# Kernel optimization log

Hardware: AMD Instinct MI355X
Metric: run time of the kernel (lower is better)

## Reference

```python
import jax, jax.numpy as jnp
import numpy as np

IN_DIM = 64
HIDDEN = 128
NUM_LAYERS = 2
N_NODES = 10000
N_EDGES = 160000
N_GRAPHS = 32


def _lin_params(key, fan_in, fan_out):
    kw, kb = jax.random.split(key)
    s = 1.0 / np.sqrt(fan_in)
    W = jax.random.uniform(kw, (fan_in, fan_out), jnp.float32, -s, s)
    b = jax.random.uniform(kb, (fan_out,), jnp.float32, -s, s)
    return W, b


def setup_inputs() -> dict:
    key = jax.random.key(0)
    ks = jax.random.split(key, 24)
    H = HIDDEN
    inp = {}
    inp["x1"] = jax.random.normal(ks[0], (N_NODES, IN_DIM), jnp.float32)
    inp["edge_index1"] = jax.random.randint(ks[1], (2, N_EDGES), 0, N_NODES)
    inp["batch1"] = jnp.sort(jax.random.randint(ks[2], (N_NODES,), 0, N_GRAPHS))
    inp["x2"] = jax.random.normal(ks[3], (N_NODES, IN_DIM), jnp.float32)
    inp["edge_index2"] = jax.random.randint(ks[4], (2, N_EDGES), 0, N_NODES)
    inp["batch2"] = jnp.sort(jax.random.randint(ks[5], (N_NODES,), 0, N_GRAPHS))
    # embedding: Linear(in_dim -> hidden)
    inp["W_emb"], inp["b_emb"] = _lin_params(ks[6], IN_DIM, H)
    # per-layer GEMBConv params, stacked over layers
    mW1, mb1, mW2, mb2, uW1, ub1, uW2, ub2 = [], [], [], [], [], [], [], []
    for l in range(NUM_LAYERS):
        k = jax.random.split(ks[7 + l], 4)
        W, b = _lin_params(k[0], 2 * H, 2 * H); mW1.append(W); mb1.append(b)
        W, b = _lin_params(k[1], 2 * H, 2 * H); mW2.append(W); mb2.append(b)
        W, b = _lin_params(k[2], 3 * H, 2 * H); uW1.append(W); ub1.append(b)
        W, b = _lin_params(k[3], 2 * H, H); uW2.append(W); ub2.append(b)
    inp["msg_W1"] = jnp.stack(mW1); inp["msg_b1"] = jnp.stack(mb1)
    inp["msg_W2"] = jnp.stack(mW2); inp["msg_b2"] = jnp.stack(mb2)
    inp["upd_W1"] = jnp.stack(uW1); inp["upd_b1"] = jnp.stack(ub1)
    inp["upd_W2"] = jnp.stack(uW2); inp["upd_b2"] = jnp.stack(ub2)
    # readout: node_net Linear(H -> 2H) (use_gate doubles), graph_net Linear(H -> H)
    inp["node_W"], inp["node_b"] = _lin_params(ks[20], H, 2 * H)
    inp["graph_W"], inp["graph_b"] = _lin_params(ks[21], H, H)
    return inp


def _genet_branch(x, edge_index, batch, W_emb, b_emb,
                  msg_W1, msg_b1, msg_W2, msg_b2,
                  upd_W1, upd_b1, upd_W2, upd_b2,
                  node_W, node_b, graph_W, graph_b):
    H = HIDDEN
    h = x @ W_emb + b_emb  # [N, H]
    tgt, src = edge_index[0], edge_index[1]
    for l in range(NUM_LAYERS):
        # gather-concat: (x[src], x[tgt]) -> [E, 2H]
        mi = jnp.concatenate([h[src], h[tgt]], axis=-1)
        m = jax.nn.relu(mi @ msg_W1[l] + msg_b1[l]) @ msg_W2[l] + msg_b2[l]
        agg = jax.ops.segment_sum(m, tgt, num_segments=N_NODES)  # [N, 2H]
        ui = jnp.concatenate([agg, h], axis=-1)  # [N, 3H]
        u = jax.nn.relu(ui @ upd_W1[l] + upd_b1[l]) @ upd_W2[l] + upd_b2[l]
        h = h + u  # residual node update
    nx = h @ node_W + node_b  # [N, 2H]
    gates = jax.nn.sigmoid(nx[:, :H])
    v = nx[:, H:] * gates
    g = jax.ops.segment_sum(v, batch, num_segments=N_GRAPHS)  # sum pool
    return g @ graph_W + graph_b  # [G, H]


def reference(x1, edge_index1, batch1, x2, edge_index2, batch2,
              W_emb, b_emb, msg_W1, msg_b1, msg_W2, msg_b2,
              upd_W1, upd_b1, upd_W2, upd_b2,
              node_W, node_b, graph_W, graph_b):
    args = (W_emb, b_emb, msg_W1, msg_b1, msg_W2, msg_b2,
            upd_W1, upd_b1, upd_W2, upd_b2, node_W, node_b, graph_W, graph_b)
    embed1 = _genet_branch(x1, edge_index1, batch1, *args)
    embed2 = _genet_branch(x2, edge_index2, batch2, *args)
    return (embed1, embed2)
```

## Files before the change

### kernel.cpp

```cpp
#include <hip/hip_runtime.h>

typedef unsigned short u16;
typedef __bf16 bf16x8 __attribute__((ext_vector_type(8)));
typedef float f32x4 __attribute__((ext_vector_type(4)));
typedef unsigned short u16x8 __attribute__((ext_vector_type(8)));

constexpr int NN  = 10000;
constexpr int NE  = 160000;
constexpr int NG  = 32;
constexpr int HD  = 128;

constexpr size_t WT_PQ   = 0;
constexpr size_t WT_U1C  = 262144;
constexpr size_t WT_UPD2 = 655360;
constexpr size_t WT_NODE = 786432;
constexpr size_t WT_EMB  = 851968;
constexpr size_t OFF_C2  = 868352;
constexpr size_t OFF_DEG = 870400;
constexpr size_t OFF_ST  = 950400;
constexpr size_t OFF_CUR = 1030464;
constexpr size_t OFF_SRC = 1110464;
constexpr size_t OFF_HB  = 2390464;
constexpr size_t OFF_PQ  = 7510464;
constexpr size_t OFF_S   = 27990464;
constexpr size_t OFF_G   = 38230464;
constexpr size_t OFF_XB  = 38263232;

#define LSTR 40

__device__ inline u16 f2b(float f) {
  unsigned int u = __float_as_uint(f);
  unsigned int r = u + 0x7fffu + ((u >> 16) & 1u);
  return (u16)(r >> 16);
}
__device__ inline float b2f(u16 u) { return __uint_as_float(((unsigned int)u) << 16); }

__global__ __launch_bounds__(256) void k_prep(
    const float* msgW1, const float* msgW2, const float* updW1,
    const float* updW2, const float* nodeW, const float* msgb2,
    const float* W_emb, const float* x1, const float* x2,
    u16* tpq, u16* tu1c, u16* t4, u16* t5, u16* temb, u16* xb,
    float* c2, int* deg, float* g) {
  int idx = blockIdx.x * 256 + threadIdx.x;
  if (idx < 131072) {
    int l = idx >> 16, r = idx & 65535, n = r >> 7, k = r & 127;
    int row = (n < 256) ? k : (128 + k);
    tpq[idx] = f2b(msgW1[l * 65536 + row * 256 + (n & 255)]);
  }
  if (idx < 65536) {
    int l = idx >> 15, r = idx & 32767, n = r >> 7, k = r & 127;
    tu1c[l * 98304 + n * 384 + 256 + k] = f2b(updW1[l * 98304 + (256 + k) * 256 + n]);
    int n2 = (idx & 32767) >> 8, k2 = idx & 255;
    t4[idx] = f2b(updW2[(idx >> 15) * 32768 + (k2 << 7) + n2]);
  }
  if (idx < 32768) {
    int n = idx >> 7, k = idx & 127;
    t5[idx] = f2b(nodeW[(k << 8) + n]);
  }
  if (idx < 512) {
    int l = idx >> 8, n = idx & 255;
    const float* b2 = msgb2 + l * 256;
    const float* U1 = updW1 + l * 98304 + n;
    float a = 0.f;
    for (int c = 0; c < 256; c++) a += b2[c] * U1[c * 256];
    c2[idx] = a;
  }
  if (idx < 2 * NN) deg[idx] = 0;
  if (idx < 2 * NG * 128) g[idx] = 0.f;
  if (idx >= 131072 && idx < 262144) {
    int j = idx - 131072;
    int l = j >> 16, r = j & 65535, k = r >> 8, n = r & 255;
    const float* w2p = msgW2 + l * 65536 + k * 256;
    const float* u1p = updW1 + l * 98304 + n;
    float a = 0.f;
    for (int c = 0; c < 256; c++) a += w2p[c] * u1p[c * 256];
    tu1c[l * 98304 + n * 384 + k] = f2b(a);
  }
  if (idx >= 262144 && idx < 270336) {
    int j = idx - 262144;
    int n = j >> 6, k = j & 63;
    temb[j] = f2b(W_emb[(k << 7) + n]);
  }
  if (idx >= 270336 && idx < 1550336) {
    int j = idx - 270336;
    int br = j >= NN * 64;
    int jj = br ? j - NN * 64 : j;
    const float* x = br ? x2 : x1;
    xb[(size_t)br * NN * 64 + jj] = f2b(x[jj]);
  }
}

__global__ __launch_bounds__(256) void k_deg(const int* ei0, const int* ei1, int* deg) {
  int br = blockIdx.z;
  int e = blockIdx.x * 256 + threadIdx.x;
  if (e >= NE) return;
  const int* tgt = br ? ei1 : ei0;
  atomicAdd(deg + br * NN + tgt[e], 1);
}

__global__ __launch_bounds__(256) void k_scan(const int* deg, int* starts, int* cursor) {
  int br = blockIdx.z;
  const int* d = deg + br * NN;
  int* st = starts + br * (NN + 8);
  int* cu = cursor + br * NN;
  __shared__ int part[257];
  int t = threadIdx.x;
  int c0 = t * 40;
  int s = 0;
  for (int i = 0; i < 40; i++) if (c0 + i < NN) s += d[c0 + i];
  part[t] = s;
  __syncthreads();
  if (t == 0) {
    int run = 0;
    for (int i = 0; i < 256; i++) { int v = part[i]; part[i] = run; run += v; }
    part[256] = run;
  }
  __syncthreads();
  int run = part[t];
  for (int i = 0; i < 40; i++) {
    int n = c0 + i;
    if (n < NN) { st[n] = run; cu[n] = run; run += d[n]; }
  }
  if (t == 255) st[NN] = part[256];
}

__global__ __launch_bounds__(256) void k_scatter(const int* ei0, const int* ei1,
                                                 int* cursor, int* srcs) {
  int br = blockIdx.z;
  int e = blockIdx.x * 256 + threadIdx.x;
  if (e >= NE) return;
  const int* ei = br ? ei1 : ei0;
  int t = ei[e], s = ei[NE + e];
  int pos = atomicAdd(cursor + br * NN + t, 1);
  srcs[br * NE + pos] = s;
}

__device__ __forceinline__ void pq_from_lhb(
    const u16* lhb, const u16* wq, u16* PQ, int m0, int wave, int lane) {
  const int q = lane >> 4, lr = lane & 15;
  f32x4 a3[2][8];
#pragma unroll
  for (int i = 0; i < 2; i++)
#pragma unroll
    for (int j = 0; j < 8; j++) a3[i][j] = (f32x4){0.f, 0.f, 0.f, 0.f};
  bf16x8 bcur[8], bnxt[8];
#pragma unroll
  for (int i = 0; i < 8; i++)
    bcur[i] = *(const bf16x8*)(wq + (size_t)(wave * 128 + i * 16 + lr) * 128 + q * 8);
#pragma unroll
  for (int k0 = 0; k0 < 128; k0 += 32) {
    if (k0 + 32 < 128) {
#pragma unroll
      for (int i = 0; i < 8; i++)
        bnxt[i] = *(const bf16x8*)(wq + (size_t)(wave * 128 + i * 16 + lr) * 128 + k0 + 32 + q * 8);
    }
    bf16x8 af[2];
#pragma unroll
    for (int i = 0; i < 2; i++)
      af[i] = *(const bf16x8*)&lhb[(i * 16 + lr) * 136 + k0 + q * 8];
#pragma unroll
    for (int mi = 0; mi < 2; mi++)
#pragma unroll
      for (int ni = 0; ni < 8; ni++)
        a3[mi][ni] = __builtin_amdgcn_mfma_f32_16x16x32_bf16(af[mi], bcur[ni], a3[mi][ni], 0, 0, 0);
#pragma unroll
    for (int i = 0; i < 8; i++) bcur[i] = bnxt[i];
  }
#pragma unroll
  for (int mi = 0; mi < 2; mi++)
#pragma unroll
    for (int rg = 0; rg < 4; rg++) {
      int grow = m0 + mi * 16 + q * 4 + rg;
      if (grow >= NN) continue;
#pragma unroll
      for (int ni = 0; ni < 8; ni++) {
        int col = wave * 128 + ni * 16 + lr;
        PQ[(size_t)grow * 512 + col] = f2b(a3[mi][ni][rg]);
      }
    }
}

__global__ __launch_bounds__(256) void k_embed(
    const u16* xb_all, const u16* wemb, const float* b,
    u16* hb_all, const u16* wpq0, u16* PQ_all) {
  const int br = blockIdx.z;
  const int tid = threadIdx.x;
  const int lane = tid & 63, wave = tid >> 6;
  const int q = lane >> 4, lr = lane & 15;
  const int m0 = blockIdx.x * 32;

  __shared__ alignas(16) u16 lx[32 * 72];
  __shared__ alignas(16) u16 lhb[32 * 136];

  const u16* xb = xb_all + (size_t)br * NN * 64;
  {
    int r = tid >> 3, kc = (tid & 7) * 8;
    int gr = m0 + r;
    u16x8 v = {0, 0, 0, 0, 0, 0, 0, 0};
    if (gr < NN) v = *(const u16x8*)(xb + (size_t)gr * 64 + kc);
    *(u16x8*)&lx[r * 72 + kc] = v;
  }
  __syncthreads();

  const int wn = wave * 32;
  f32x4 acc[2][2];
#pragma unroll
  for (int i = 0; i < 2; i++)
#pragma unroll
    for (int j = 0; j < 2; j++) acc[i][j] = (f32x4){0.f, 0.f, 0.f, 0.f};

#pragma unroll
  for (int k0 = 0; k0 < 64; k0 += 32) {
    bf16x8 af[2], bfr[2];
#pragma unroll
    for (int i = 0; i < 2; i++)
      af[i] = *(const bf16x8*)&lx[(i * 16 + lr) * 72 + k0 + q * 8];
#pragma unroll
    for (int i = 0; i < 2; i++)
      bfr[i] = *(const bf16x8*)(wemb + (size_t)(wn + i * 16 + lr) * 64 + k0 + q * 8);
#pragma unroll
    for (int mi = 0; mi < 2; mi++)
#pragma unroll
      for (int ni = 0; ni < 2; ni++)
        acc[mi][ni] = __builtin_amdgcn_mfma_f32_16x16x32_bf16(af[mi], bfr[ni], acc[mi][ni], 0, 0, 0);
  }

  u16* hbB = hb_all + (size_t)br * NN * HD;
#pragma unroll
  for (int mi = 0; mi < 2; mi++)
#pragma unroll
    for (int rg = 0; rg < 4; rg++) {
      int lrow = mi * 16 + q * 4 + rg;
      int gr = m0 + lrow;
#pragma unroll
      for (int ni = 0; ni < 2; ni++) {
        int col = wn + ni * 16 + lr;
        if (gr < NN) {
          u16 bv = f2b(acc[mi][ni][rg] + b[col]);
          hbB[(size_t)gr * HD + col] = bv;
          lhb[lrow * 136 + col] = bv;
        } else {
          lhb[lrow * 136 + col] = 0;
        }
      }
    }
  __syncthreads();
  pq_from_lhb(lhb, wpq0, PQ_all + (size_t)br * NN * 512, m0, wave, lane);
}

__global__ __launch_bounds__(256) void k_edge(const u16* PQ, const int* starts,
                                              const int* srcs, const float* b1, u16* S) {
  int br = blockIdx.z;
  int node = blockIdx.x * 4 + (threadIdx.x >> 6);
  int lane = threadIdx.x & 63;
  int half = lane >> 5;
  int c0 = (lane & 31) * 8;
  const u16* PQb = PQ + (size_t)br * NN * 512;
  const int* st = starts + br * (NN + 8);
  const int* sr = srcs + br * NE;
  u16x8 qr = *(const u16x8*)(PQb + (size_t)node * 512 + 256 + c0);
  float qv[8], acc[8];
#pragma unroll
  for (int j = 0; j < 8; j++) { qv[j] = b2f(qr[j]) + b1[c0 + j]; acc[j] = 0.f; }
  int e0 = st[node], e1 = st[node + 1];
  int mid = e0 + ((e1 - e0 + 1) >> 1);
  int e = half ? mid : e0;
  int ee = half ? e1 : mid;
  for (; e + 3 < ee; e += 4) {
    int s0 = sr[e], s1 = sr[e + 1], s2 = sr[e + 2], s3 = sr[e + 3];
    u16x8 p0 = *(const u16x8*)(PQb + (size_t)s0 * 512 + c0);
    u16x8 p1 = *(const u16x8*)(PQb + (size_t)s1 * 512 + c0);
    u16x8 p2 = *(const u16x8*)(PQb + (size_t)s2 * 512 + c0);
    u16x8 p3 = *(const u16x8*)(PQb + (size_t)s3 * 512 + c0);
#pragma unroll
    for (int j = 0; j < 8; j++) {
      float v0 = b2f(p0[j]) + qv[j];
      float v1 = b2f(p1[j]) + qv[j];
      float v2 = b2f(p2[j]) + qv[j];
      float v3 = b2f(p3[j]) + qv[j];
      acc[j] += (v0 > 0.f ? v0 : 0.f) + (v1 > 0.f ? v1 : 0.f)
              + (v2 > 0.f ? v2 : 0.f) + (v3 > 0.f ? v3 : 0.f);
    }
  }
  for (; e + 1 < ee; e += 2) {
    int s0 = sr[e], s1 = sr[e + 1];
    u16x8 p0 = *(const u16x8*)(PQb + (size_t)s0 * 512 + c0);
    u16x8 p1 = *(const u16x8*)(PQb + (size_t)s1 * 512 + c0);
#pragma unroll
    for (int j = 0; j < 8; j++) {
      float v0 = b2f(p0[j]) + qv[j];
      float v1 = b2f(p1[j]) + qv[j];
      acc[j] += (v0 > 0.f ? v0 : 0.f) + (v1 > 0.f ? v1 : 0.f);
    }
  }
  if (e < ee) {
    int s0 = sr[e];
    u16x8 p0 = *(const u16x8*)(PQb + (size_t)s0 * 512 + c0);
#pragma unroll
    for (int j = 0; j < 8; j++) {
      float v0 = b2f(p0[j]) + qv[j];
      acc[j] += (v0 > 0.f ? v0 : 0.f);
    }
  }
#pragma unroll
  for (int j = 0; j < 8; j++) acc[j] += __shfl_xor(acc[j], 32);
  if (half == 0) {
    u16x8 o;
#pragma unroll
    for (int j = 0; j < 8; j++) o[j] = f2b(acc[j]);
    *(u16x8*)(S + (size_t)br * NN * 256 + (size_t)node * 256 + c0) = o;
  }
}

__global__ __launch_bounds__(256, 4) void k_upd(
    const u16* S_all, u16* hb_all, const u16* w1c, const float* b1u,
    const float* c2l, const int* deg_all, const u16* w2, const float* b2u,
    int mode, const u16* wpq_next, u16* PQ_all,
    const u16* wnode, const float* nb, const int* b0v, const int* b1v, float* g) {
  const int br = blockIdx.z;
  const int tid = threadIdx.x;
  const int lane = tid & 63, wave = tid >> 6;
  const int q = lane >> 4, lr = lane & 15;
  const int m0 = blockIdx.x * 32;

  __shared__ alignas(16) u16 lA[32 * 392];
  __shared__ alignas(16) u16 lhb[32 * 136];
  __shared__ int sbat[32];
  u16* lU = lA;

  const u16* S = S_all + (size_t)br * NN * 256;
  u16* hb = hb_all + (size_t)br * NN * 128;

  for (int c = tid; c < 1536; c += 256) {
    int r = c / 48, kc = (c % 48) * 8;
    int gr = m0 + r;
    u16x8 v = {0, 0, 0, 0, 0, 0, 0, 0};
    if (gr < NN) {
      if (kc < 256) v = *(const u16x8*)(S + (size_t)gr * 256 + kc);
      else          v = *(const u16x8*)(hb + (size_t)gr * 128 + (kc - 256));
    }
    *(u16x8*)&lA[r * 392 + kc] = v;
  }
  if (mode == 1 && tid < 32) {
    const int* batch = br ? b1v : b0v;
    int n = m0 + tid;
    sbat[tid] = (n < NN) ? batch[n] : -1;
  }
  __syncthreads();

  const int wn = wave * 64;
  f32x4 acc[2][4];
#pragma unroll
  for (int i = 0; i < 2; i++)
#pragma unroll
    for (int j = 0; j < 4; j++) acc[i][j] = (f32x4){0.f, 0.f, 0.f, 0.f};

  bf16x8 bcur[4], bnxt[4];
#pragma unroll
  for (int i = 0; i < 4; i++)
    bcur[i] = *(const bf16x8*)(w1c + (size_t)(wn + i * 16 + lr) * 384 + q * 8);
#pragma unroll
  for (int k0 = 0; k0 < 384; k0 += 32) {
    if (k0 + 32 < 384) {
#pragma unroll
      for (int i = 0; i < 4; i++)
        bnxt[i] = *(const bf16x8*)(w1c + (size_t)(wn + i * 16 + lr) * 384 + k0 + 32 + q * 8);
    }
    bf16x8 af[2];
#pragma unroll
    for (int i = 0; i < 2; i++)
      af[i] = *(const bf16x8*)&lA[(i * 16 + lr) * 392 + k0 + q * 8];
#pragma unroll
    for (int mi = 0; mi < 2; mi++)
#pragma unroll
      for (int ni = 0; ni < 4; ni++)
        acc[mi][ni] = __builtin_amdgcn_mfma_f32_16x16x32_bf16(af[mi], bcur[ni], acc[mi][ni], 0, 0, 0);
#pragma unroll
    for (int i = 0; i < 4; i++) bcur[i] = bnxt[i];
  }
  __syncthreads();

  const int* deg = deg_all + br * NN;
#pragma unroll
  for (int mi = 0; mi < 2; mi++)
#pragma unroll
    for (int rg = 0; rg < 4; rg++) {
      int row = mi * 16 + q * 4 + rg;
      int gr = m0 + row;
      float d = (gr < NN) ? (float)deg[gr] : 0.f;
#pragma unroll
      for (int ni = 0; ni < 4; ni++) {
        int col = wn + ni * 16 + lr;
        float v = acc[mi][ni][rg] + b1u[col] + d * c2l[col];
        if (v < 0.f) v = 0.f;
        lU[row * 272 + col] = f2b(v);
      }
    }
  __syncthreads();

  const int wn2 = wave * 32;
  f32x4 acc2[2][2];
#pragma unroll
  for (int i = 0; i < 2; i++)
#pragma unroll
    for (int j = 0; j < 2; j++) acc2[i][j] = (f32x4){0.f, 0.f, 0.f, 0.f};

  bf16x8 b2c[2], b2n[2];
#pragma unroll
  for (int i = 0; i < 2; i++)
    b2c[i] = *(const bf16x8*)(w2 + (size_t)(wn2 + i * 16 + lr) * 256 + q * 8);
#pragma unroll
  for (int k0 = 0; k0 < 256; k0 += 32) {
    if (k0 + 32 < 256) {
#pragma unroll
      for (int i = 0; i < 2; i++)
        b2n[i] = *(const bf16x8*)(w2 + (size_t)(wn2 + i * 16 + lr) * 256 + k0 + 32 + q * 8);
    }
    bf16x8 af[2];
#pragma unroll
    for (int i = 0; i < 2; i++)
      af[i] = *(const bf16x8*)&lU[(i * 16 + lr) * 272 + k0 + q * 8];
#pragma unroll
    for (int mi = 0; mi < 2; mi++)
#pragma unroll
      for (int ni = 0; ni < 2; ni++)
        acc2[mi][ni] = __builtin_amdgcn_mfma_f32_16x16x32_bf16(af[mi], b2c[ni], acc2[mi][ni], 0, 0, 0);
#pragma unroll
    for (int i = 0; i < 2; i++) b2c[i] = b2n[i];
  }

#pragma unroll
  for (int mi = 0; mi < 2; mi++)
#pragma unroll
    for (int rg = 0; rg < 4; rg++) {
      int lrow = mi * 16 + q * 4 + rg;
      int grow = m0 + lrow;
#pragma unroll
      for (int ni = 0; ni < 2; ni++) {
        int col = wn2 + ni * 16 + lr;
        if (grow < NN) {
          size_t o = (size_t)grow * 128 + col;
          float nh = b2f(hb[o]) + acc2[mi][ni][rg] + b2u[col];
          u16 bv = f2b(nh);
          hb[o] = bv;
          lhb[lrow * 136 + col] = bv;
        } else {
          lhb[lrow * 136 + col] = 0;
        }
      }
    }
  __syncthreads();

  if (mode == 0) {
    pq_from_lhb(lhb, wpq_next, PQ_all + (size_t)br * NN * 512, m0, wave, lane);
  } else {
    const int wg = wave * 32;
    f32x4 a3[2][4];
#pragma unroll
    for (int i = 0; i < 2; i++)
#pragma unroll
      for (int j = 0; j < 4; j++) a3[i][j] = (f32x4){0.f, 0.f, 0.f, 0.f};
#pragma unroll
    for (int k0 = 0; k0 < 128; k0 += 32) {
      bf16x8 af[2], bfr[4];
#pragma unroll
      for (int i = 0; i < 2; i++)
        af[i] = *(const bf16x8*)&lhb[(i * 16 + lr) * 136 + k0 + q * 8];
#pragma unroll
      for (int i = 0; i < 4; i++) {
        int nrow = (i < 2) ? (wg + i * 16 + lr) : (128 + wg + (i - 2) * 16 + lr);
        bfr[i] = *(const bf16x8*)(wnode + (size_t)nrow * 128 + k0 + q * 8);
      }
#pragma unroll
      for (int mi = 0; mi < 2; mi++)
#pragma unroll
        for (int ni = 0; ni < 4; ni++)
          a3[mi][ni] = __builtin_amdgcn_mfma_f32_16x16x32_bf16(af[mi], bfr[ni], a3[mi][ni], 0, 0, 0);
    }
    float* gb = g + (size_t)br * NG * 128;
    float racc[2] = {0.f, 0.f};
    int cur = -1;
#pragma unroll
    for (int mi = 0; mi < 2; mi++)
#pragma unroll
      for (int rg = 0; rg < 4; rg++) {
        int lrow = mi * 16 + q * 4 + rg;
        int bt = sbat[lrow];
        if (bt != cur) {
          if (cur >= 0) {
#pragma unroll
            for (int ni = 0; ni < 2; ni++)
              atomicAdd(gb + (size_t)cur * 128 + wg + ni * 16 + lr, racc[ni]);
          }
          cur = bt;
          racc[0] = 0.f; racc[1] = 0.f;
        }
        if (bt >= 0) {
#pragma unroll
          for (int ni = 0; ni < 2; ni++) {
            int gcol = wg + ni * 16 + lr;
            float gt = a3[mi][ni][rg] + nb[gcol];
            float vl = a3[mi][ni + 2][rg] + nb[128 + gcol];
            racc[ni] += vl / (1.f + __expf(-gt));
          }
        }
      }
    if (cur >= 0) {
#pragma unroll
      for (int ni = 0; ni < 2; ni++)
        atomicAdd(gb + (size_t)cur * 128 + wg + ni * 16 + lr, racc[ni]);
    }
  }
}

__global__ __launch_bounds__(128) void k_final(const float* g, const float* W,
                                               const float* b, float* out) {
  int br = blockIdx.z, gi = blockIdx.x, j = threadIdx.x;
  __shared__ float sg[128];
  sg[j] = g[(size_t)br * NG * 128 + (size_t)gi * 128 + j];
  __syncthreads();
  float acc = b[j];
#pragma unroll
  for (int k = 0; k < 128; k++) acc += sg[k] * W[k * 128 + j];
  out[(size_t)br * NG * 128 + (size_t)gi * 128 + j] = acc;
}

extern "C" void kernel_launch(void* const* d_in, const int* in_sizes, int n_in,
                              void* d_out, int out_size, void* d_ws, size_t ws_size,
                              hipStream_t stream) {
  const float* x1     = (const float*)d_in[0];
  const int*   ei1    = (const int*)d_in[1];
  const int*   bat1   = (const int*)d_in[2];
  const float* x2     = (const float*)d_in[3];
  const int*   ei2    = (const int*)d_in[4];
  const int*   bat2   = (const int*)d_in[5];
  const float* W_emb  = (const float*)d_in[6];
  const float* b_emb  = (const float*)d_in[7];
  const float* msg_W1 = (const float*)d_in[8];
  const float* msg_b1 = (const float*)d_in[9];
  const float* msg_W2 = (const float*)d_in[10];
  const float* msg_b2 = (const float*)d_in[11];
  const float* upd_W1 = (const float*)d_in[12];
  const float* upd_b1 = (const float*)d_in[13];
  const float* upd_W2 = (const float*)d_in[14];
  const float* upd_b2 = (const float*)d_in[15];
  const float* node_W = (const float*)d_in[16];
  const float* node_b = (const float*)d_in[17];
  const float* graph_W = (const float*)d_in[18];
  const float* graph_b = (const float*)d_in[19];
  float* out = (float*)d_out;

  char* ws = (char*)d_ws;
  u16* wt_pq   = (u16*)(ws + WT_PQ);
  u16* wt_u1c  = (u16*)(ws + WT_U1C);
  u16* wt_upd2 = (u16*)(ws + WT_UPD2);
  u16* wt_node = (u16*)(ws + WT_NODE);
  u16* wt_emb  = (u16*)(ws + WT_EMB);
  float* c2    = (float*)(ws + OFF_C2);
  int* deg    = (int*)(ws + OFF_DEG);
  int* starts = (int*)(ws + OFF_ST);
  int* cursor = (int*)(ws + OFF_CUR);
  int* srcs   = (int*)(ws + OFF_SRC);
  u16* hb     = (u16*)(ws + OFF_HB);
  u16* PQ     = (u16*)(ws + OFF_PQ);
  u16* S      = (u16*)(ws + OFF_S);
  float* g    = (float*)(ws + OFF_G);
  u16* xb     = (u16*)(ws + OFF_XB);

  k_prep<<<6057, 256, 0, stream>>>(msg_W1, msg_W2, upd_W1, upd_W2, node_W, msg_b2,
                                   W_emb, x1, x2,
                                   wt_pq, wt_u1c, wt_upd2, wt_node, wt_emb, xb,
                                   c2, deg, g);
  k_deg<<<dim3(625, 1, 2), 256, 0, stream>>>(ei1, ei2, deg);
  k_scan<<<dim3(1, 1, 2), 256, 0, stream>>>(deg, starts, cursor);
  k_scatter<<<dim3(625, 1, 2), 256, 0, stream>>>(ei1, ei2, cursor, srcs);
  k_embed<<<dim3(313, 1, 2), 256, 0, stream>>>(xb, wt_emb, b_emb, hb, wt_pq, PQ);

  for (int l = 0; l < 2; l++) {
    k_edge<<<dim3(2500, 1, 2), 256, 0, stream>>>(PQ, starts, srcs, msg_b1 + l * 256, S);

    k_upd<<<dim3(313, 1, 2), 256, 0, stream>>>(
        S, hb, wt_u1c + (size_t)l * 98304, upd_b1 + l * 256, c2 + l * 256,
        deg, wt_upd2 + (size_t)l * 32768, upd_b2 + l * 128,
        (l == 0) ? 0 : 1,
        wt_pq + 65536, PQ,
        wt_node, node_b, bat1, bat2, g);
  }

  k_final<<<dim3(NG, 1, 2), 128, 0, stream>>>(g, graph_W, graph_b, out);
}
```

Measured before the change: 331.9 us.

## Halve k_upd row tile to 16 nodes and double its grid

The node-update kernel now processes 16 rows per block instead of 32 and launches 625 blocks per branch instead of 313, for more parallelism across CUs. Bounds checks are dropped because 10000 divides evenly by 16. The old hidden state is read from shared memory rather than global, and the PQ projection for the next layer is inlined with register double-buffered weight loads. In exchange, each block reloads the full weight matrices while covering half as many rows, which doubles weight traffic per node.

Result: slower. 368.7 us (+11.1%).

```diff
diff --git a/kernel.cpp b/kernel.cpp
--- a/kernel.cpp
+++ b/kernel.cpp
@@ -321,39 +321,35 @@
   const int tid = threadIdx.x;
   const int lane = tid & 63, wave = tid >> 6;
   const int q = lane >> 4, lr = lane & 15;
-  const int m0 = blockIdx.x * 32;
-
-  __shared__ alignas(16) u16 lA[32 * 392];
-  __shared__ alignas(16) u16 lhb[32 * 136];
-  __shared__ int sbat[32];
+  const int m0 = blockIdx.x * 16;
+
+  __shared__ alignas(16) u16 lA[16 * 392];
+  __shared__ alignas(16) u16 lhb[16 * 136];
+  __shared__ int sbat[16];
   u16* lU = lA;
 
   const u16* S = S_all + (size_t)br * NN * 256;
   u16* hb = hb_all + (size_t)br * NN * 128;
 
-  for (int c = tid; c < 1536; c += 256) {
+  for (int c = tid; c < 768; c += 256) {
     int r = c / 48, kc = (c % 48) * 8;
     int gr = m0 + r;
-    u16x8 v = {0, 0, 0, 0, 0, 0, 0, 0};
-    if (gr < NN) {
-      if (kc < 256) v = *(const u16x8*)(S + (size_t)gr * 256 + kc);
-      else          v = *(const u16x8*)(hb + (size_t)gr * 128 + (kc - 256));
-    }
+    u16x8 v;
+    if (kc < 256) v = *(const u16x8*)(S + (size_t)gr * 256 + kc);
+    else          v = *(const u16x8*)(hb + (size_t)gr * 128 + (kc - 256));
     *(u16x8*)&lA[r * 392 + kc] = v;
   }
-  if (mode == 1 && tid < 32) {
+  if (mode == 1 && tid < 16) {
     const int* batch = br ? b1v : b0v;
-    int n = m0 + tid;
-    sbat[tid] = (n < NN) ? batch[n] : -1;
+    sbat[tid] = batch[m0 + tid];
   }
   __syncthreads();
 
   const int wn = wave * 64;
-  f32x4 acc[2][4];
-#pragma unroll
-  for (int i = 0; i < 2; i++)
-#pragma unroll
-    for (int j = 0; j < 4; j++) acc[i][j] = (f32x4){0.f, 0.f, 0.f, 0.f};
+  const int wn2 = wave * 32;
+  f32x4 acc[4];
+#pragma unroll
+  for (int j = 0; j < 4; j++) acc[j] = (f32x4){0.f, 0.f, 0.f, 0.f};
 
   bf16x8 bcur[4], bnxt[4];
 #pragma unroll
@@ -366,44 +362,40 @@
       for (int i = 0; i < 4; i++)
         bnxt[i] = *(const bf16x8*)(w1c + (size_t)(wn + i * 16 + lr) * 384 + k0 + 32 + q * 8);
     }
-    bf16x8 af[2];
-#pragma unroll
-    for (int i = 0; i < 2; i++)
-      af[i] = *(const bf16x8*)&lA[(i * 16 + lr) * 392 + k0 + q * 8];
-#pragma unroll
-    for (int mi = 0; mi < 2; mi++)
-#pragma unroll
-      for (int ni = 0; ni < 4; ni++)
-        acc[mi][ni] = __builtin_amdgcn_mfma_f32_16x16x32_bf16(af[mi], bcur[ni], acc[mi][ni], 0, 0, 0);
+    bf16x8 af = *(const bf16x8*)&lA[lr * 392 + k0 + q * 8];
+#pragma unroll
+    for (int ni = 0; ni < 4; ni++)
+      acc[ni] = __builtin_amdgcn_mfma_f32_16x16x32_bf16(af, bcur[ni], acc[ni], 0, 0, 0);
 #pragma unroll
     for (int i = 0; i < 4; i++) bcur[i] = bnxt[i];
   }
+
+  float oldh[4][2];
+#pragma unroll
+  for (int rg = 0; rg < 4; rg++)
+#pragma unroll
+    for (int ni = 0; ni < 2; ni++)
+      oldh[rg][ni] = b2f(lA[(q * 4 + rg) * 392 + 256 + wn2 + ni * 16 + lr]);
   __syncthreads();
 
   const int* deg = deg_all + br * NN;
 #pragma unroll
-  for (int mi = 0; mi < 2; mi++)
-#pragma unroll
-    for (int rg = 0; rg < 4; rg++) {
-      int row = mi * 16 + q * 4 + rg;
-      int gr = m0 + row;
-      float d = (gr < NN) ? (float)deg[gr] : 0.f;
-#pragma unroll
-      for (int ni = 0; ni < 4; ni++) {
-        int col = wn + ni * 16 + lr;
-        float v = acc[mi][ni][rg] + b1u[col] + d * c2l[col];
-        if (v < 0.f) v = 0.f;
-        lU[row * 272 + col] = f2b(v);
-      }
-    }
-  __syncthreads();
-
-  const int wn2 = wave * 32;
-  f32x4 acc2[2][2];
-#pragma unroll
-  for (int i = 0; i < 2; i++)
-#pragma unroll
-    for (int j = 0; j < 2; j++) acc2[i][j] = (f32x4){0.f, 0.f, 0.f, 0.f};
+  for (int rg = 0; rg < 4; rg++) {
+    int row = q * 4 + rg;
+    float d = (float)deg[m0 + row];
+#pragma unroll
+    for (int ni = 0; ni < 4; ni++) {
+      int col = wn + ni * 16 + lr;
+      float v = acc[ni][rg] + b1u[col] + d * c2l[col];
+      if (v < 0.f) v = 0.f;
+      lU[row * 272 + col] = f2b(v);
+    }
+  }
+  __syncthreads();
+
+  f32x4 acc2[2];
+#pragma unroll
+  for (int j = 0; j < 2; j++) acc2[j] = (f32x4){0.f, 0.f, 0.f, 0.f};
 
   bf16x8 b2c[2], b2n[2];
 #pragma unroll
@@ -416,95 +408,103 @@
       for (int i = 0; i < 2; i++)
         b2n[i] = *(const bf16x8*)(w2 + (size_t)(wn2 + i * 16 + lr) * 256 + k0 + 32 + q * 8);
     }
-    bf16x8 af[2];
-#pragma unroll
-    for (int i = 0; i < 2; i++)
-      af[i] = *(const bf16x8*)&lU[(i * 16 + lr) * 272 + k0 + q * 8];
-#pragma unroll
-    for (int mi = 0; mi < 2; mi++)
-#pragma unroll
-      for (int ni = 0; ni < 2; ni++)
-        acc2[mi][ni] = __builtin_amdgcn_mfma_f32_16x16x32_bf16(af[mi], b2c[ni], acc2[mi][ni], 0, 0, 0);
+    bf16x8 af = *(const bf16x8*)&lU[lr * 272 + k0 + q * 8];
+#pragma unroll
+    for (int ni = 0; ni < 2; ni++)
+      acc2[ni] = __builtin_amdgcn_mfma_f32_16x16x32_bf16(af, b2c[ni], acc2[ni], 0, 0, 0);
 #pragma unroll
     for (int i = 0; i < 2; i++) b2c[i] = b2n[i];
   }
 
 #pragma unroll
-  for (int mi = 0; mi < 2; mi++)
+  for (int rg = 0; rg < 4; rg++) {
+    int lrow = q * 4 + rg;
+    int grow = m0 + lrow;
+#pragma unroll
+    for (int ni = 0; ni < 2; ni++) {
+      int col = wn2 + ni * 16 + lr;
+      float nh = oldh[rg][ni] + acc2[ni][rg] + b2u[col];
+      u16 bv = f2b(nh);
+      hb[(size_t)grow * 128 + col] = bv;
+      lhb[lrow * 136 + col] = bv;
+    }
+  }
+  __syncthreads();
+
+  if (mode == 0) {
+    u16* PQ = PQ_all + (size_t)br * NN * 512;
+    f32x4 a3[8];
+#pragma unroll
+    for (int j = 0; j < 8; j++) a3[j] = (f32x4){0.f, 0.f, 0.f, 0.f};
+    bf16x8 pcur[8], pnxt[8];
+#pragma unroll
+    for (int i = 0; i < 8; i++)
+      pcur[i] = *(const bf16x8*)(wpq_next + (size_t)(wave * 128 + i * 16 + lr) * 128 + q * 8);
+#pragma unroll
+    for (int k0 = 0; k0 < 128; k0 += 32) {
+      if (k0 + 32 < 128) {
+#pragma unroll
+        for (int i = 0; i < 8; i++)
+          pnxt[i] = *(const bf16x8*)(wpq_next + (size_t)(wave * 128 + i * 16 + lr) * 128 + k0 + 32 + q * 8);
+      }
+      bf16x8 af = *(const bf16x8*)&lhb[lr * 136 + k0 + q * 8];
+#pragma unroll
+      for (int ni = 0; ni < 8; ni++)
+        a3[ni] = __builtin_amdgcn_mfma_f32_16x16x32_bf16(af, pcur[ni], a3[ni], 0, 0, 0);
+#pragma unroll
+      for (int i = 0; i < 8; i++) pcur[i] = pnxt[i];
+    }
 #pragma unroll
     for (int rg = 0; rg < 4; rg++) {
-      int lrow = mi * 16 + q * 4 + rg;
-      int grow = m0 + lrow;
-#pragma unroll
-      for (int ni = 0; ni < 2; ni++) {
-        int col = wn2 + ni * 16 + lr;
-        if (grow < NN) {
-          size_t o = (size_t)grow * 128 + col;
-          float nh = b2f(hb[o]) + acc2[mi][ni][rg] + b2u[col];
-          u16 bv = f2b(nh);
-          hb[o] = bv;
-          lhb[lrow * 136 + col] = bv;
-        } else {
-          lhb[lrow * 136 + col] = 0;
-        }
-      }
-    }
-  __syncthreads();
-
-  if (mode == 0) {
-    pq_from_lhb(lhb, wpq_next, PQ_all + (size_t)br * NN * 512, m0, wave, lane);
+      int grow = m0 + q * 4 + rg;
+#pragma unroll
+      for (int ni = 0; ni < 8; ni++) {
+        int col = wave * 128 + ni * 16 + lr;
+        PQ[(size_t)grow * 512 + col] = f2b(a3[ni][rg]);
+      }
+    }
   } else {
     const int wg = wave * 32;
-    f32x4 a3[2][4];
-#pragma unroll
-    for (int i = 0; i < 2; i++)
-#pragma unroll
-      for (int j = 0; j < 4; j++) a3[i][j] = (f32x4){0.f, 0.f, 0.f, 0.f};
+    f32x4 a3[4];
+#pragma unroll
+    for (int j = 0; j < 4; j++) a3[j] = (f32x4){0.f, 0.f, 0.f, 0.f};
 #pragma unroll
     for (int k0 = 0; k0 < 128; k0 += 32) {
-      bf16x8 af[2], bfr[4];
-#pragma unroll
-      for (int i = 0; i < 2; i++)
-        af[i] = *(const bf16x8*)&lhb[(i * 16 + lr) * 136 + k0 + q * 8];
+      bf16x8 af = *(const bf16x8*)&lhb[lr * 136 + k0 + q * 8];
+      bf16x8 bfr[4];
 #pragma unroll
       for (int i = 0; i < 4; i++) {
         int nrow = (i < 2) ? (wg + i * 16 + lr) : (128 + wg + (i - 2) * 16 + lr);
         bfr[i] = *(const bf16x8*)(wnode + (size_t)nrow * 128 + k0 + q * 8);
       }
 #pragma unroll
-      for (int mi = 0; mi < 2; mi++)
-#pragma unroll
-        for (int ni = 0; ni < 4; ni++)
-          a3[mi][ni] = __builtin_amdgcn_mfma_f32_16x16x32_bf16(af[mi], bfr[ni], a3[mi][ni], 0, 0, 0);
+      for (int ni = 0; ni < 4; ni++)
+        a3[ni] = __builtin_amdgcn_mfma_f32_16x16x32_bf16(af, bfr[ni], a3[ni], 0, 0, 0);
     }
     float* gb = g + (size_t)br * NG * 128;
     float racc[2] = {0.f, 0.f};
     int cur = -1;
 #pragma unroll
-    for (int mi = 0; mi < 2; mi++)
-#pragma unroll
-      for (int rg = 0; rg < 4; rg++) {
-        int lrow = mi * 16 + q * 4 + rg;
-        int bt = sbat[lrow];
-        if (bt != cur) {
-          if (cur >= 0) {
-#pragma unroll
-            for (int ni = 0; ni < 2; ni++)
-              atomicAdd(gb + (size_t)cur * 128 + wg + ni * 16 + lr, racc[ni]);
-          }
-          cur = bt;
-          racc[0] = 0.f; racc[1] = 0.f;
+    for (int rg = 0; rg < 4; rg++) {
+      int lrow = q * 4 + rg;
+      int bt = sbat[lrow];
+      if (bt != cur) {
+        if (cur >= 0) {
+#pragma unroll
+          for (int ni = 0; ni < 2; ni++)
+            atomicAdd(gb + (size_t)cur * 128 + wg + ni * 16 + lr, racc[ni]);
         }
-        if (bt >= 0) {
-#pragma unroll
-          for (int ni = 0; ni < 2; ni++) {
-            int gcol = wg + ni * 16 + lr;
-            float gt = a3[mi][ni][rg] + nb[gcol];
-            float vl = a3[mi][ni + 2][rg] + nb[128 + gcol];
-            racc[ni] += vl / (1.f + __expf(-gt));
-          }
-        }
-      }
+        cur = bt;
+        racc[0] = 0.f; racc[1] = 0.f;
+      }
+#pragma unroll
+      for (int ni = 0; ni < 2; ni++) {
+        int gcol = wg + ni * 16 + lr;
+        float gt = a3[ni][rg] + nb[gcol];
+        float vl = a3[ni + 2][rg] + nb[128 + gcol];
+        racc[ni] += vl / (1.f + __expf(-gt));
+      }
+    }
     if (cur >= 0) {
 #pragma unroll
       for (int ni = 0; ni < 2; ni++)
@@ -579,7 +579,7 @@
   for (int l = 0; l < 2; l++) {
     k_edge<<<dim3(2500, 1, 2), 256, 0, stream>>>(PQ, starts, srcs, msg_b1 + l * 256, S);
 
-    k_upd<<<dim3(313, 1, 2), 256, 0, stream>>>(
+    k_upd<<<dim3(625, 1, 2), 256, 0, stream>>>(
         S, hb, wt_u1c + (size_t)l * 98304, upd_b1 + l * 256, c2 + l * 256,
         deg, wt_upd2 + (size_t)l * 32768, upd_b2 + l * 128,
         (l == 0) ? 0 : 1,
```
